# Performance work log

Measured on AMD Instinct MI355X. Metric: run time of the kernel, lower is better.

The kernel has to match this reference:

```python
import jax, jax.numpy as jnp
import numpy as np

LOG2PI = float(np.log(2.0 * np.pi))
VAR = 1e-4
LOGVAR = float(np.log(VAR))


def _gauss_lp(x, mean, dim):
    # MVN log_prob with covariance VAR * I_dim
    sq = jnp.sum((x - mean) ** 2, axis=-1)
    return -0.5 * (dim * (LOG2PI + LOGVAR) + sq / VAR)


def setup_inputs() -> dict:
    B, T, D, H, K = 32, 512, 256, 512, 8
    key = jax.random.key(0)
    ks = jax.random.split(key, 20)
    s = 0.05
    return {
        "x_input": jax.random.normal(ks[0], (B, T, D), jnp.float32),
        "y_train": jax.random.normal(ks[1], (B, T, D), jnp.float32),
        "sampled_h": jax.random.normal(ks[2], (B, T, H), jnp.float32),
        "initials": jax.random.normal(ks[3], (K,), jnp.float32),
        # per-state single-layer RNNs (tanh), weights [K,H,D]/[K,H,H]
        "Wih": jax.random.normal(ks[4], (K, H, D), jnp.float32) * s,
        "Whh": jax.random.normal(ks[5], (K, H, H), jnp.float32) * s,
        "bih": jax.random.normal(ks[6], (K, H), jnp.float32) * s,
        "bhh": jax.random.normal(ks[7], (K, H), jnp.float32) * s,
        # transition RNNCell (h0=0, so only input path + both biases matter)
        "Wt_ih": jax.random.normal(ks[8], (K * K, H), jnp.float32) * s,
        "bt": jax.random.normal(ks[9], (K * K,), jnp.float32) * s,
        # Emission MLP H -> 32 -> 64 -> D
        "W1": jax.random.normal(ks[10], (32, H), jnp.float32) * s,
        "b1": jax.random.normal(ks[11], (32,), jnp.float32) * s,
        "W2": jax.random.normal(ks[12], (64, 32), jnp.float32) * s,
        "b2": jax.random.normal(ks[13], (64,), jnp.float32) * s,
        "W3": jax.random.normal(ks[14], (D, 64), jnp.float32) * s,
        "b3": jax.random.normal(ks[15], (D,), jnp.float32) * s,
    }


def reference(x_input, y_train, sampled_h, initials, Wih, Whh, bih, bhh,
              Wt_ih, bt, W1, b1, W2, b2, W3, b3):
    B, T, D = x_input.shape
    H = sampled_h.shape[-1]
    K = initials.shape[0]
    lse = jax.scipy.special.logsumexp

    # initial log-probs (same for every batch row)
    prob_initial = jnp.broadcast_to(initials - lse(initials), (B, K))

    # ---- prob_all_h: per-state RNN step log-likelihoods ----
    h_prev = sampled_h[:, :-1]  # [B,T-1,H]
    pre = (jnp.einsum('btd,khd->btkh', x_input[:, 1:], Wih)
           + jnp.einsum('bth,kgh->btkg', h_prev, Whh)
           + bih[None, None] + bhh[None, None])  # [B,T-1,K,H]
    x_out = jnp.tanh(pre)
    lp_rest = _gauss_lp(sampled_h[:, 1:, None, :], x_out, H)  # [B,T-1,K]
    lp0 = -0.5 * H * (LOG2PI + LOGVAR)  # log_prob of the mean itself at t=0
    prob_all_h = jnp.concatenate(
        [jnp.full((B, 1, K), lp0, jnp.float32), lp_rest], axis=1)  # [B,T,K]

    # ---- prob_all_s: transition log-probs (normalized over axis=2) ----
    trans = jnp.tanh(jnp.einsum('bth,ch->btc', h_prev, Wt_ih) + bt)
    trans = trans.reshape(B, T - 1, K, K)
    s_rest = trans - lse(trans, axis=2, keepdims=True)
    s0 = jnp.broadcast_to(jnp.eye(K, dtype=jnp.float32), (B, 1, K, K))
    prob_all_s = jnp.concatenate([s0, s_rest], axis=1)  # [B,T,K,K]

    # ---- prob_all_y: emission MLP + MVN log-prob ----
    h1 = jax.nn.relu(sampled_h @ W1.T + b1)
    h2 = jax.nn.relu(h1 @ W2.T + b2)
    em = h2 @ W3.T + b3  # [B,T,D]
    prob_all_y = _gauss_lp(y_train, em, D)  # [B,T]

    log_e = prob_all_h + prob_all_y[..., None]  # [B,T,K]

    # ---- forward pass (Baum-Welch alpha, log-space) ----
    s_tm = jnp.swapaxes(prob_all_s[:, 1:], 0, 1)  # [T-1,B,K,K]
    e_tm = jnp.swapaxes(log_e[:, 1:], 0, 1)       # [T-1,B,K]
    alpha0 = prob_initial + log_e[:, 0]

    def fstep(a, xs):
        s_t, e_t = xs
        a_new = e_t + lse(a[:, None, :] + s_t, axis=2)  # s[b,i,j]=logp(i|j)
        return a_new, a_new

    _, alphas = jax.lax.scan(fstep, alpha0, (s_tm, e_tm))
    forward_prob = jnp.concatenate(
        [alpha0[:, None], jnp.swapaxes(alphas, 0, 1)], axis=1)  # [B,T,K]

    # ---- backward pass (beta) ----
    betaT = jnp.zeros((B, K), jnp.float32)

    def bstep(b, xs):
        s_t1, e_t1 = xs
        b_new = lse(s_t1 + (e_t1 + b)[:, :, None], axis=1)
        return b_new, b_new

    _, betas = jax.lax.scan(bstep, betaT, (s_tm, e_tm), reverse=True)
    backward_prob = jnp.concatenate(
        [jnp.swapaxes(betas, 0, 1), betaT[:, None]], axis=1)  # [B,T,K]

    # ---- gammas ----
    ab = forward_prob + backward_prob
    gamma1 = ab - lse(ab, axis=2, keepdims=True)  # [B,T,K]
    pair = (forward_prob[:, :-1, None, :] + prob_all_s[:, 1:]
            + (log_e[:, 1:] + backward_prob[:, 1:])[:, :, :, None])
    gamma2 = pair - lse(pair, axis=(2, 3), keepdims=True)  # [B,T-1,K,K]

    return (prob_initial, prob_all_s, prob_all_h, prob_all_y,
            gamma1, gamma2, forward_prob, backward_prob)
```

## Files before the change

kernel.cpp:

```cpp
#include <hip/hip_runtime.h>

typedef _Float16 f16;
typedef _Float16 f16x8 __attribute__((ext_vector_type(8)));
typedef float f32x16 __attribute__((ext_vector_type(16)));

#define NB 32
#define NT 512
#define ND 256
#define NH 512
#define M_REAL 16352
#define RDIM 768
#define TILE_ELEMS 98304
#define NTN 33

#define OFF_PI 0
#define OFF_S  256
#define OFF_H  1048832
#define OFF_Y  1179904
#define OFF_G1 1196288
#define OFF_G2 1327360
#define OFF_F  2373888
#define OFF_BW 2504960

#define WS_A    0
#define WS_B    25165824
#define WS_BIAS 31653888
#define WS_SQ   31671296
#define WS_M    33768448
#define WS_NEED 34292736

#define CH_CONST 1887.3506062251f
#define CY_CONST 943.6753031126f
#define LOG2E 1.4426950408889634f
#define LN2 0.6931471805599453f
#define NEGINF -1e30f

#define CA_BLOCKS 1024
#define CB_BLOCKS 264
#define CONV_GRID 1288

__device__ __forceinline__ float fexp2(float x) { return __builtin_amdgcn_exp2f(x); }
__device__ __forceinline__ float flog2(float x) { return __builtin_amdgcn_logf(x); }
__device__ __forceinline__ float ftanh(float x) {
    x = fminf(10.f, fmaxf(-10.f, x));
    float t = fexp2(x * 2.885390081777927f);
    return (t - 1.f) * __builtin_amdgcn_rcpf(t + 1.f);
}
__device__ __forceinline__ float lse8v(const float* z) {
    float M = fmaxf(fmaxf(fmaxf(z[0], z[1]), fmaxf(z[2], z[3])),
                    fmaxf(fmaxf(z[4], z[5]), fmaxf(z[6], z[7])));
    const float e0 = fexp2((z[0] - M) * LOG2E), e1 = fexp2((z[1] - M) * LOG2E);
    const float e2 = fexp2((z[2] - M) * LOG2E), e3 = fexp2((z[3] - M) * LOG2E);
    const float e4 = fexp2((z[4] - M) * LOG2E), e5 = fexp2((z[5] - M) * LOG2E);
    const float e6 = fexp2((z[6] - M) * LOG2E), e7 = fexp2((z[7] - M) * LOG2E);
    const float s = ((e0 + e1) + (e2 + e3)) + ((e4 + e5) + (e6 + e7));
    return M + LN2 * flog2(s);
}

__global__ __launch_bounds__(256) void conv_ab_kernel(
    const float* __restrict__ x, const float* __restrict__ h,
    const float* __restrict__ Wih, const float* __restrict__ Whh,
    const float* __restrict__ bih, const float* __restrict__ bhh,
    const float* __restrict__ Wt, const float* __restrict__ btv,
    f16* __restrict__ A, f16* __restrict__ Bm, float* __restrict__ biasc) {
    __shared__ __align__(16) f16x8 tb[16 * 97];
    const int tid = threadIdx.x;
    if (blockIdx.x < CA_BLOCKS) {
        const int m0 = blockIdx.x * 16;
#pragma unroll
        for (int i = 0; i < 6; ++i) {
            const int idx = tid + 256 * i;
            const int ml = idx / 96;
            const int ch = idx - ml * 96;
            const int m = m0 + ml;
            f16x8 pk = (f16x8)(f16)0.f;
            if (m < M_REAL) {
                const int b = m / 511;
                const int t = m - b * 511;
                const int c0 = ch * 8;
                const float* src = (c0 < ND) ? x + (size_t)(b * NT + t + 1) * ND + c0
                                             : h + (size_t)(b * NT + t) * NH + (c0 - ND);
                const float4 u = ((const float4*)src)[0];
                const float4 v = ((const float4*)src)[1];
                pk[0] = (f16)u.x; pk[1] = (f16)u.y; pk[2] = (f16)u.z; pk[3] = (f16)u.w;
                pk[4] = (f16)v.x; pk[5] = (f16)v.y; pk[6] = (f16)v.z; pk[7] = (f16)v.w;
            }
            tb[ml * 97 + ch] = pk;
        }
        __syncthreads();
        const size_t tbase = (size_t)(m0 >> 7) * TILE_ELEMS + (size_t)(m0 & 127) * 8;
#pragma unroll
        for (int i = 0; i < 6; ++i) {
            const int idx = tid + 256 * i;
            const int ch2 = idx >> 4;
            const int m2 = idx & 15;
            *(f16x8*)(A + tbase + (size_t)ch2 * 1024 + (size_t)m2 * 8) = tb[m2 * 97 + ch2];
        }
    } else {
        const int n0 = (blockIdx.x - CA_BLOCKS) * 16;
#pragma unroll
        for (int i = 0; i < 6; ++i) {
            const int idx = tid + 256 * i;
            const int nl = idx / 96;
            const int ch = idx - nl * 96;
            const int n = n0 + nl;
            const int c0 = ch * 8;
            f16x8 pk = (f16x8)(f16)0.f;
            const float* src = nullptr;
            if (n < 4096) {
                src = (c0 < ND) ? Wih + (size_t)n * ND + c0 : Whh + (size_t)n * NH + (c0 - ND);
            } else {
                const int c = n - 4096;
                if (c < 64 && c0 >= ND) src = Wt + (size_t)c * NH + (c0 - ND);
            }
            if (src) {
                const float4 u = ((const float4*)src)[0];
                const float4 v = ((const float4*)src)[1];
                pk[0] = (f16)u.x; pk[1] = (f16)u.y; pk[2] = (f16)u.z; pk[3] = (f16)u.w;
                pk[4] = (f16)v.x; pk[5] = (f16)v.y; pk[6] = (f16)v.z; pk[7] = (f16)v.w;
            }
            tb[nl * 97 + ch] = pk;
        }
        if (tid < 16) {
            const int n = n0 + tid;
            biasc[n] = (n < 4096) ? bih[n] + bhh[n] : ((n - 4096) < 64 ? btv[n - 4096] : 0.f);
        }
        __syncthreads();
        const size_t tbase = (size_t)(n0 >> 7) * TILE_ELEMS + (size_t)(n0 & 127) * 8;
#pragma unroll
        for (int i = 0; i < 6; ++i) {
            const int idx = tid + 256 * i;
            const int ch2 = idx >> 4;
            const int m2 = idx & 15;
            *(f16x8*)(Bm + tbase + (size_t)ch2 * 1024 + (size_t)m2 * 8) = tb[m2 * 97 + ch2];
        }
    }
}

__global__ __launch_bounds__(256) void emission_kernel(
    const float* __restrict__ h, const float* __restrict__ y,
    const float* __restrict__ W1, const float* __restrict__ b1,
    const float* __restrict__ W2, const float* __restrict__ b2,
    const float* __restrict__ W3, const float* __restrict__ b3,
    float* __restrict__ out) {
    __shared__ __align__(16) float smem[11904];
    const int tid = threadIdx.x;
    float* ssh = smem;
    float* W2sh = smem + 8192;
    float* h1sh = smem + 10304;
    float* h2sh = smem + 10816;
    float* red = smem + 11840;
    const int wv = tid >> 6;
    const int o = tid >> 3, seg = tid & 7;
    const int p0 = blockIdx.x * 16;
    float4 w1r[16], w3r[16];
    {
        const float4* w1p = (const float4*)(W1 + (size_t)o * NH + seg * 64);
#pragma unroll
        for (int j = 0; j < 16; ++j) w1r[j] = w1p[(j + seg * 2) & 15];
        const float4* w3p = (const float4*)(W3 + (size_t)tid * 64);
#pragma unroll
        for (int j = 0; j < 16; ++j) w3r[j] = w3p[j];
    }
    if (tid < 64) {
        for (int j = 0; j < 32; ++j) W2sh[tid * 33 + j] = W2[tid * 32 + j];
    }
    float yv[16];
#pragma unroll
    for (int pp = 0; pp < 16; ++pp) yv[pp] = y[(size_t)(p0 + pp) * ND + tid];
    const float b1r = b1[o];
    const float b2r = b2[tid & 63];
    const float b3r = b3[tid];
#pragma unroll
    for (int pp = 0; pp < 16; ++pp) {
        const float2 hv = ((const float2*)(h + (size_t)(p0 + pp) * NH))[tid];
        ssh[pp * 512 + tid * 2] = hv.x;
        ssh[pp * 512 + tid * 2 + 1] = hv.y;
    }
    __syncthreads();
#pragma unroll
    for (int pp = 0; pp < 16; ++pp) {
        const float4* s4 = (const float4*)&ssh[pp * 512 + seg * 64];
        float p = 0.f;
#pragma unroll
        for (int it = 0; it < 16; ++it) {
            const float4 sv = s4[(it + seg * 2) & 15];
            const float4 w = w1r[it];
            p += w.x * sv.x + w.y * sv.y + w.z * sv.z + w.w * sv.w;
        }
        p += __shfl_xor(p, 1, 64);
        p += __shfl_xor(p, 2, 64);
        p += __shfl_xor(p, 4, 64);
        if (seg == 0) h1sh[pp * 32 + o] = fmaxf(p + b1r, 0.f);
    }
    __syncthreads();
    {
        const int o2 = tid & 63;
#pragma unroll
        for (int it = 0; it < 4; ++it) {
            const int pp = wv * 4 + it;
            float s = b2r;
#pragma unroll
            for (int j = 0; j < 32; ++j) s += W2sh[o2 * 33 + j] * h1sh[pp * 32 + j];
            h2sh[pp * 64 + o2] = fmaxf(s, 0.f);
        }
    }
    __syncthreads();
#pragma unroll
    for (int pp = 0; pp < 16; ++pp) {
        float s = b3r;
        const float4* h24 = (const float4*)&h2sh[pp * 64];
#pragma unroll
        for (int j = 0; j < 16; ++j) {
            const float4 w = w3r[j], hb = h24[j];
            s += w.x * hb.x + w.y * hb.y + w.z * hb.z + w.w * hb.w;
        }
        const float d = yv[pp] - s;
        float sq = d * d;
#pragma unroll
        for (int off = 32; off > 0; off >>= 1) sq += __shfl_xor(sq, off, 64);
        if ((tid & 63) == 0) red[pp * 4 + wv] = sq;
    }
    __syncthreads();
    if (tid < 16) {
        out[OFF_Y + p0 + tid] =
            CY_CONST - 5000.f * (red[tid * 4] + red[tid * 4 + 1] + red[tid * 4 + 2] +
                                 red[tid * 4 + 3]);
    }
}

__global__ __launch_bounds__(256) void gemm_kernel(const f16* __restrict__ A,
                                                   const f16* __restrict__ Bm,
                                                   const float* __restrict__ biasc,
                                                   const float* __restrict__ sampled_h,
                                                   float* __restrict__ sq_part,
                                                   float* __restrict__ Ps) {
    __shared__ __align__(16) f16 Ash[8 * 128 * 8];
    __shared__ __align__(16) f16 Bsh[8 * 128 * 8];
    const int tid = threadIdx.x;
    const int lane = tid & 63;
    const int wave = tid >> 6;
    const int xcd = blockIdx.x & 7;
    const int slot = blockIdx.x >> 3;
    const int tm = xcd * 16 + slot / NTN;
    const int tn = slot % NTN;
    const int m0 = tm * 128, n0 = tn * 128;
    const int l31 = lane & 31, hk = lane >> 5;

    f32x16 acc[4];
#pragma unroll
    for (int a = 0; a < 4; ++a) acc[a] = (f32x16)0.f;

    for (int kk = 0; kk < RDIM; kk += 64) {
        __syncthreads();
        const size_t abase = (size_t)tm * TILE_ELEMS + (size_t)kk * 128;
        const size_t bbase = (size_t)tn * TILE_ELEMS + (size_t)kk * 128;
#pragma unroll
        for (int inst = 0; inst < 4; ++inst) {
            const int fb = inst * 256 + wave * 64;
            const f16* ga = A + abase + (size_t)(fb + lane) * 8;
            const f16* gb = Bm + bbase + (size_t)(fb + lane) * 8;
            __builtin_amdgcn_global_load_lds(
                (const __attribute__((address_space(1))) void*)ga,
                (__attribute__((address_space(3))) void*)&Ash[fb * 8], 16, 0, 0);
            __builtin_amdgcn_global_load_lds(
                (const __attribute__((address_space(1))) void*)gb,
                (__attribute__((address_space(3))) void*)&Bsh[fb * 8], 16, 0, 0);
        }
        __syncthreads();
#pragma unroll
        for (int kc = 0; kc < 4; ++kc) {
            const int ch = kc * 2 + hk;
            const f16x8 af = *(const f16x8*)&Ash[(ch * 128 + wave * 32 + l31) * 8];
            f16x8 bfr[4];
#pragma unroll
            for (int ni = 0; ni < 4; ++ni)
                bfr[ni] = *(const f16x8*)&Bsh[(ch * 128 + ni * 32 + l31) * 8];
#pragma unroll
            for (int ni = 0; ni < 4; ++ni)
                acc[ni] = __builtin_amdgcn_mfma_f32_32x32x16_f16(af, bfr[ni], acc[ni], 0, 0, 0);
        }
    }

    if (tn == 32) {
        const float bt0 = biasc[4096 + l31];
        const float bt1 = biasc[4096 + 32 + l31];
#pragma unroll
        for (int r = 0; r < 16; ++r) {
            const int mg = m0 + wave * 32 + (r & 3) + 8 * (r >> 2) + 4 * hk;
            if (mg < M_REAL) {
                const float v0 = ftanh(acc[0][r] + bt0);
                const float v1 = ftanh(acc[1][r] + bt1);
                float M = fmaxf(v0, v1);
                M = fmaxf(M, __shfl_xor(M, 8, 64));
                M = fmaxf(M, __shfl_xor(M, 16, 64));
                float s = fexp2((v0 - M) * LOG2E) + fexp2((v1 - M) * LOG2E);
                s += __shfl_xor(s, 8, 64);
                s += __shfl_xor(s, 16, 64);
                const float lse = M + LN2 * flog2(s);
                const int b = mg / 511, t = mg - b * 511;
                const size_t base = (size_t)(b * NT + t + 1) * 64;
                Ps[base + l31] = v0 - lse;
                Ps[base + 32 + l31] = v1 - lse;
            }
        }
    } else {
        const int k0 = n0 >> 9;
        const int slot4 = (n0 >> 7) & 3;
        const float b0 = biasc[n0 + l31];
        const float b1v = biasc[n0 + 32 + l31];
        const float b2v = biasc[n0 + 64 + l31];
        const float b3v = biasc[n0 + 96 + l31];
#pragma unroll
        for (int r = 0; r < 16; ++r) {
            const int mg = m0 + wave * 32 + (r & 3) + 8 * (r >> 2) + 4 * hk;
            if (mg < M_REAL) {
                const int bb = mg / 511;
                const int tt = mg - bb * 511;
                const float* tgt = sampled_h + (size_t)((bb << 9) + tt + 1) * NH;
                const float d0 = tgt[(n0 + l31) & 511] - ftanh(acc[0][r] + b0);
                const float d1 = tgt[(n0 + 32 + l31) & 511] - ftanh(acc[1][r] + b1v);
                const float d2 = tgt[(n0 + 64 + l31) & 511] - ftanh(acc[2][r] + b2v);
                const float d3 = tgt[(n0 + 96 + l31) & 511] - ftanh(acc[3][r] + b3v);
                float rs = d0 * d0 + d1 * d1 + d2 * d2 + d3 * d3;
                rs += __shfl_xor(rs, 1, 64);
                rs += __shfl_xor(rs, 2, 64);
                rs += __shfl_xor(rs, 4, 64);
                rs += __shfl_xor(rs, 8, 64);
                rs += __shfl_xor(rs, 16, 64);
                if (l31 == 0) sq_part[(size_t)(mg * 8 + k0) * 4 + slot4] = rs;
            }
        }
    }
}

__global__ void post_kernel(const float* __restrict__ sq_part,
                            const float* __restrict__ initials, float* __restrict__ out) {
    const int g = blockIdx.x * 256 + threadIdx.x;
    const int b = g >> 12;
    const int t = (g >> 3) & 511;
    const int k = g & 7;
    float val;
    if (t == 0) {
        val = CH_CONST;
    } else {
        const int m = b * 511 + (t - 1);
        const float4 a = *(const float4*)&sq_part[(size_t)(m * 8 + k) * 4];
        val = CH_CONST - 5000.f * (a.x + a.y + a.z + a.w);
    }
    out[OFF_H + g] = val;
    if (g < 2048) {
        const int sb = g >> 6, c = g & 63;
        out[OFF_S + (size_t)sb * NT * 64 + c] = ((c >> 3) == (c & 7)) ? 1.f : 0.f;
    }
    if (g < 256) {
        float z[8];
#pragma unroll
        for (int j = 0; j < 8; ++j) z[j] = initials[j];
        out[OFF_PI + g] = z[g & 7] - lse8v(z);
    }
}


template <bool WRITE>
__device__ __forceinline__ float fwd_run(const float* __restrict__ Ps,
                                         const float* __restrict__ Ph,
                                         const float* __restrict__ Py,
                                         float* __restrict__ Fw, int b, int t0,
                                         int t1, float a, int lane) {
    const int i = lane & 7;
    const int base = lane & ~7;
    float4 cA[8], cB[8], nA[8], nB[8];
    float cH[8], cY[8], nH[8], nY[8];
#define FLOADR(G, A_, B_, H_, Y_)                                              \
    _Pragma("unroll") for (int jj = 0; jj < 8; ++jj) {                         \
        int t = t0 + (G) * 8 + jj;                                             \
        t = t > t1 ? t1 : t;                                                   \
        const size_t p = (size_t)(b * NT + t) * 64 + i * 8;                    \
        A_[jj] = *(const float4*)&Ps[p];                                       \
        B_[jj] = *(const float4*)&Ps[p + 4];                                   \
        H_[jj] = Ph[(size_t)(b * NT + t) * 8 + i];                             \
        Y_[jj] = Py[b * NT + t];                                               \
    }
#define FSTEPR(G, A_, B_, H_, Y_)                                              \
    _Pragma("unroll") for (int jj = 0; jj < 8; ++jj) {                         \
        const int t = t0 + (G) * 8 + jj;                                       \
        if (t <= t1) {                                                         \
            float z[8];                                                        \
            z[0] = __shfl(a, base + 0, 64) + A_[jj].x;                         \
            z[1] = __shfl(a, base + 1, 64) + A_[jj].y;                         \
            z[2] = __shfl(a, base + 2, 64) + A_[jj].z;                         \
            z[3] = __shfl(a, base + 3, 64) + A_[jj].w;                         \
            z[4] = __shfl(a, base + 4, 64) + B_[jj].x;                         \
            z[5] = __shfl(a, base + 5, 64) + B_[jj].y;                         \
            z[6] = __shfl(a, base + 6, 64) + B_[jj].z;                         \
            z[7] = __shfl(a, base + 7, 64) + B_[jj].w;                         \
            a = (H_[jj] + Y_[jj]) + lse8v(z);                                  \
            if (WRITE && lane < 8) Fw[(size_t)(b * NT + t) * 8 + i] = a;       \
        }                                                                      \
    }
    FLOADR(0, cA, cB, cH, cY);
    FLOADR(1, nA, nB, nH, nY);
    FSTEPR(0, cA, cB, cH, cY);
    FLOADR(2, cA, cB, cH, cY);
    FSTEPR(1, nA, nB, nH, nY);
    FLOADR(3, nA, nB, nH, nY);
    FSTEPR(2, cA, cB, cH, cY);
    FSTEPR(3, nA, nB, nH, nY);
#undef FLOADR
#undef FSTEPR
    return a;
}

template <bool WRITE>
__device__ __forceinline__ float bwd_run(const float* __restrict__ Ps,
                                         const float* __restrict__ Ph,
                                         const float* __restrict__ Py,
                                         float* __restrict__ Bw, int b, int tt0,
                                         int tt1, float a, int lane) {
    const int i = lane & 7;
    const int base = lane & ~7;
    float cS[8][8], nS[8][8], cH[8], cY[8], nH[8], nY[8];
#define BLOADR(G, S_, H_, Y_)                                                  \
    _Pragma("unroll") for (int jj = 0; jj < 8; ++jj) {                         \
        int t = tt0 - (G) * 8 - jj;                                            \
        t = t < tt1 ? tt1 : t;                                                 \
        const size_t q = (size_t)(b * NT + t + 1);                             \
        _Pragma("unroll") for (int ii = 0; ii < 8; ++ii)                       \
            S_[jj][ii] = Ps[q * 64 + ii * 8 + i];                              \
        H_[jj] = Ph[q * 8 + i];                                                \
        Y_[jj] = Py[q];                                                       \
    }
#define BSTEPR(G, S_, H_, Y_)                                                  \
    _Pragma("unroll") for (int jj = 0; jj < 8; ++jj) {                         \
        const int t = tt0 - (G) * 8 - jj;                                      \
        if (t >= tt1) {                                                        \
            const float v = H_[jj] + Y_[jj] + a;                               \
            float z[8];                                                        \
            _Pragma("unroll") for (int ii = 0; ii < 8; ++ii)                   \
                z[ii] = __shfl(v, base + ii, 64) + S_[jj][ii];                 \
            a = lse8v(z);                                                      \
            if (WRITE && lane < 8) Bw[(size_t)(b * NT + t) * 8 + i] = a;       \
        }                                                                      \
    }
    BLOADR(0, cS, cH, cY);
    BLOADR(1, nS, nH, nY);
    BSTEPR(0, cS, cH, cY);
    BLOADR(2, cS, cH, cY);
    BSTEPR(1, nS, nH, nY);
    BLOADR(3, nS, nH, nY);
    BSTEPR(2, cS, cH, cY);
    BSTEPR(3, nS, nH, nY);
#undef BLOADR
#undef BSTEPR
    return a;
}

__global__ __launch_bounds__(256) void scan_mat_kernel(const float* __restrict__ out,
                                                       float* __restrict__ Mws) {
    const float* Ps = out + OFF_S;
    const float* Ph = out + OFF_H;
    const float* Py = out + OFF_Y;
    const int lane = threadIdx.x & 63;
    const int wave = threadIdx.x >> 6;
    const int i = lane & 7, j = lane >> 3;
    float a = (i == j) ? 0.f : NEGINF;
    if (blockIdx.x < 128) {
        const int b = blockIdx.x >> 2;
        const int c = (blockIdx.x & 3) * 4 + wave;
        const int t0 = 1 + 32 * c;
        const int t1 = (32 * (c + 1) < 511) ? 32 * (c + 1) : 511;
        a = fwd_run<false>(Ps, Ph, Py, nullptr, b, t0, t1, a, lane);
        Mws[(size_t)(b * 16 + c) * 64 + lane] = a;
    } else {
        const int b = (blockIdx.x - 128) >> 2;
        const int c = ((blockIdx.x - 128) & 3) * 4 + wave;
        const int tt0 = 510 - 32 * c;
        const int tt1 = (479 - 32 * c > 0) ? 479 - 32 * c : 0;
        a = bwd_run<false>(Ps, Ph, Py, nullptr, b, tt0, tt1, a, lane);
        Mws[32768 + (size_t)(b * 16 + c) * 64 + lane] = a;
    }
}

__global__ __launch_bounds__(256) void scan_fin_kernel(const float* __restrict__ initials,
                                                       float* __restrict__ out,
                                                       const float* __restrict__ Mws) {
    const float* Ps = out + OFF_S;
    const float* Ph = out + OFF_H;
    const float* Py = out + OFF_Y;
    const int lane = threadIdx.x & 63;
    const int wave = threadIdx.x >> 6;
    const int i = lane & 7;
    const int base = lane & ~7;
    const bool fwd = blockIdx.x < 128;
    const int blk = fwd ? blockIdx.x : blockIdx.x - 128;
    const int b = blk >> 2;
    const int c = (blk & 3) * 4 + wave;
    const float* Mbase = Mws + (fwd ? 0 : 32768) + (size_t)(b * 16) * 64;

    float a;
    if (fwd) {
        float z0[8];
#pragma unroll
        for (int jj = 0; jj < 8; ++jj) z0[jj] = initials[jj];
        a = (z0[i] - lse8v(z0)) + CH_CONST + Py[b * NT];
        if (c == 0 && lane < 8) (out + OFF_F)[(size_t)(b * NT) * 8 + i] = a;
    } else {
        a = 0.f;
        if (c == 0 && lane < 8) (out + OFF_BW)[(size_t)(b * NT + NT - 1) * 8 + i] = 0.f;
    }
    if (c > 0) {
        float4 r0 = *(const float4*)&Mbase[0 * 64 + i * 8];
        float4 r1 = *(const float4*)&Mbase[0 * 64 + i * 8 + 4];
        for (int cc = 0; cc < c; ++cc) {
            float4 s0, s1;
            if (cc + 1 < c) {
                s0 = *(const float4*)&Mbase[(size_t)(cc + 1) * 64 + i * 8];
                s1 = *(const float4*)&Mbase[(size_t)(cc + 1) * 64 + i * 8 + 4];
            }
            float z[8];
            z[0] = __shfl(a, base + 0, 64) + r0.x;
            z[1] = __shfl(a, base + 1, 64) + r0.y;
            z[2] = __shfl(a, base + 2, 64) + r0.z;
            z[3] = __shfl(a, base + 3, 64) + r0.w;
            z[4] = __shfl(a, base + 4, 64) + r1.x;
            z[5] = __shfl(a, base + 5, 64) + r1.y;
            z[6] = __shfl(a, base + 6, 64) + r1.z;
            z[7] = __shfl(a, base + 7, 64) + r1.w;
            a = lse8v(z);
            r0 = s0;
            r1 = s1;
        }
    }
    if (fwd) {
        const int t0 = 1 + 32 * c;
        const int t1 = (32 * (c + 1) < 511) ? 32 * (c + 1) : 511;
        fwd_run<true>(Ps, Ph, Py, out + OFF_F, b, t0, t1, a, lane);
    } else {
        const int tt0 = 510 - 32 * c;
        const int tt1 = (479 - 32 * c > 0) ? 479 - 32 * c : 0;
        bwd_run<true>(Ps, Ph, Py, out + OFF_BW, b, tt0, tt1, a, lane);
    }
}

__global__ void gamma_kernel(float* __restrict__ out) {
    const float* Ps = out + OFF_S;
    const float* Ph = out + OFF_H;
    const float* Py = out + OFF_Y;
    const float* Fw = out + OFF_F;
    const float* Bw = out + OFF_BW;
    if (blockIdx.x < 511) {
        const int gidx = blockIdx.x * 256 + threadIdx.x;
        const int pos = gidx >> 3;
        const int i = gidx & 7;
        const int b = pos / 511, t = pos - b * 511;
        const size_t t1 = (size_t)(b * NT + t + 1);
        const float ei = Ph[t1 * 8 + i] + Py[t1] + Bw[t1 * 8 + i];
        const float4 sa = ((const float4*)&Ps[(t1 * 8 + i) * 8])[0];
        const float4 sb = ((const float4*)&Ps[(t1 * 8 + i) * 8])[1];
        const float4 fa = ((const float4*)&Fw[(size_t)(b * NT + t) * 8])[0];
        const float4 fb = ((const float4*)&Fw[(size_t)(b * NT + t) * 8])[1];
        float z[8] = {fa.x + sa.x + ei, fa.y + sa.y + ei, fa.z + sa.z + ei, fa.w + sa.w + ei,
                      fb.x + sb.x + ei, fb.y + sb.y + ei, fb.z + sb.z + ei, fb.w + sb.w + ei};
        float M = fmaxf(fmaxf(fmaxf(z[0], z[1]), fmaxf(z[2], z[3])),
                        fmaxf(fmaxf(z[4], z[5]), fmaxf(z[6], z[7])));
        M = fmaxf(M, __shfl_xor(M, 1, 64));
        M = fmaxf(M, __shfl_xor(M, 2, 64));
        M = fmaxf(M, __shfl_xor(M, 4, 64));
        float s = 0.f;
#pragma unroll
        for (int j = 0; j < 8; ++j) s += fexp2((z[j] - M) * LOG2E);
        s += __shfl_xor(s, 1, 64);
        s += __shfl_xor(s, 2, 64);
        s += __shfl_xor(s, 4, 64);
        const float l = M + LN2 * flog2(s);
        float* G2 = out + OFF_G2;
        float4 o0 = {z[0] - l, z[1] - l, z[2] - l, z[3] - l};
        float4 o1 = {z[4] - l, z[5] - l, z[6] - l, z[7] - l};
        ((float4*)&G2[(size_t)gidx * 8])[0] = o0;
        ((float4*)&G2[(size_t)gidx * 8])[1] = o1;
    } else {
        const int pos = (blockIdx.x - 511) * 256 + threadIdx.x;
        const float4 fa = ((const float4*)&Fw[(size_t)pos * 8])[0];
        const float4 fb = ((const float4*)&Fw[(size_t)pos * 8])[1];
        const float4 ba = ((const float4*)&Bw[(size_t)pos * 8])[0];
        const float4 bb = ((const float4*)&Bw[(size_t)pos * 8])[1];
        float ab[8] = {fa.x + ba.x, fa.y + ba.y, fa.z + ba.z, fa.w + ba.w,
                       fb.x + bb.x, fb.y + bb.y, fb.z + bb.z, fb.w + bb.w};
        const float l = lse8v(ab);
        float* G1 = out + OFF_G1;
        float4 o0 = {ab[0] - l, ab[1] - l, ab[2] - l, ab[3] - l};
        float4 o1 = {ab[4] - l, ab[5] - l, ab[6] - l, ab[7] - l};
        ((float4*)&G1[(size_t)pos * 8])[0] = o0;
        ((float4*)&G1[(size_t)pos * 8])[1] = o1;
    }
}

extern "C" void kernel_launch(void* const* d_in, const int* in_sizes, int n_in, void* d_out,
                              int out_size, void* d_ws, size_t ws_size, hipStream_t stream) {
    const float* x = (const float*)d_in[0];
    const float* y = (const float*)d_in[1];
    const float* h = (const float*)d_in[2];
    const float* initials = (const float*)d_in[3];
    const float* Wih = (const float*)d_in[4];
    const float* Whh = (const float*)d_in[5];
    const float* bih = (const float*)d_in[6];
    const float* bhh = (const float*)d_in[7];
    const float* Wt = (const float*)d_in[8];
    const float* btv = (const float*)d_in[9];
    const float* W1 = (const float*)d_in[10];
    const float* b1 = (const float*)d_in[11];
    const float* W2 = (const float*)d_in[12];
    const float* b2 = (const float*)d_in[13];
    const float* W3 = (const float*)d_in[14];
    const float* b3 = (const float*)d_in[15];
    float* out = (float*)d_out;
    char* ws = (char*)d_ws;
    if (ws_size < (size_t)WS_NEED) return;
    f16* Aws = (f16*)(ws + WS_A);
    f16* Bws = (f16*)(ws + WS_B);
    float* biasc = (float*)(ws + WS_BIAS);
    float* sqp = (float*)(ws + WS_SQ);
    float* Mws = (float*)(ws + WS_M);

    conv_ab_kernel<<<CONV_GRID, 256, 0, stream>>>(x, h, Wih, Whh, bih, bhh, Wt, btv, Aws,
                                                  Bws, biasc);
    gemm_kernel<<<4224, 256, 0, stream>>>(Aws, Bws, biasc, h, sqp, out + OFF_S);
    emission_kernel<<<1024, 256, 0, stream>>>(h, y, W1, b1, W2, b2, W3, b3, out);
    post_kernel<<<512, 256, 0, stream>>>(sqp, initials, out);
    scan_mat_kernel<<<256, 256, 0, stream>>>(out, Mws);
    scan_fin_kernel<<<256, 256, 0, stream>>>(initials, out, Mws);
    gamma_kernel<<<575, 256, 0, stream>>>(out);
}
```

Before: 379.6 us.

## Enlarge GEMM tiles to 256x256 with double-buffered LDS and software-pipelined MFMA

Rewrites the main fused GEMM to use 256x256 output tiles per 512-thread block, with each wave computing a 128x64 sub-tile. Global-to-LDS loads are double-buffered and overlapped with MFMA phases, with register ping-pong of fragments and s_setprio around the MFMAs. The goal is more operand reuse per LDS load and less load latency exposed between K steps. The epilogue now reduces partial squared sums through LDS before writing. The cost is higher register and LDS pressure, and wasted MFMA work on the clamped last N tile, where only one wave column's results are used.

```diff
diff --git a/kernel.cpp b/kernel.cpp
--- a/kernel.cpp
+++ b/kernel.cpp
@@ -229,106 +229,190 @@
     }
 }
 
-__global__ __launch_bounds__(256) void gemm_kernel(const f16* __restrict__ A,
-                                                   const f16* __restrict__ Bm,
-                                                   const float* __restrict__ biasc,
-                                                   const float* __restrict__ sampled_h,
-                                                   float* __restrict__ sq_part,
-                                                   float* __restrict__ Ps) {
-    __shared__ __align__(16) f16 Ash[8 * 128 * 8];
-    __shared__ __align__(16) f16 Bsh[8 * 128 * 8];
+__global__ __launch_bounds__(512, 2) void gemm_kernel(const f16* __restrict__ A,
+                                                      const f16* __restrict__ Bm,
+                                                      const float* __restrict__ biasc,
+                                                      const float* __restrict__ sampled_h,
+                                                      float* __restrict__ sq_part,
+                                                      float* __restrict__ Ps) {
+    __shared__ __align__(16) f16 Ash[2][16384];
+    __shared__ __align__(16) f16 Bsh[2][16384];
     const int tid = threadIdx.x;
     const int lane = tid & 63;
     const int wave = tid >> 6;
+    const int wm = wave >> 2;
+    const int wn = wave & 3;
+    const int l31 = lane & 31, hk = lane >> 5;
     const int xcd = blockIdx.x & 7;
-    const int slot = blockIdx.x >> 3;
-    const int tm = xcd * 16 + slot / NTN;
-    const int tn = slot % NTN;
-    const int m0 = tm * 128, n0 = tn * 128;
-    const int l31 = lane & 31, hk = lane >> 5;
-
-    f32x16 acc[4];
-#pragma unroll
-    for (int a = 0; a < 4; ++a) acc[a] = (f32x16)0.f;
-
-    for (int kk = 0; kk < RDIM; kk += 64) {
+    const int local = blockIdx.x >> 3;
+    const int tm = xcd * 8 + local / 17;
+    const int tn = local % 17;
+    const int bt0 = 2 * tn;
+    const int bt1 = (2 * tn + 1 > 32) ? 32 : 2 * tn + 1;
+    const size_t ga0 = (size_t)(2 * tm) * TILE_ELEMS + (size_t)tid * 8;
+    const size_t ga1 = (size_t)(2 * tm + 1) * TILE_ELEMS + (size_t)tid * 8;
+    const size_t gb0 = (size_t)bt0 * TILE_ELEMS + (size_t)tid * 8;
+    const size_t gb1 = (size_t)bt1 * TILE_ELEMS + (size_t)tid * 8;
+    const int aoff = wm * 8192 + hk * 1024 + l31 * 8;
+    const int boff = (wn >> 1) * 8192 + hk * 1024 + ((wn & 1) * 64 + l31) * 8;
+
+    f32x16 acc[4][2];
+#pragma unroll
+    for (int mi = 0; mi < 4; ++mi)
+#pragma unroll
+        for (int ni = 0; ni < 2; ++ni) acc[mi][ni] = (f32x16)0.f;
+
+#define GLDS(SRC, DST) \
+    __builtin_amdgcn_global_load_lds( \
+        (const __attribute__((address_space(1))) void*)(SRC), \
+        (__attribute__((address_space(3))) void*)(DST), 16, 0, 0)
+
+#define STAGE(kt, bi) \
+    do { \
+        const size_t ko = (size_t)(kt) * 8192; \
+        GLDS(A + ga0 + ko, &Ash[bi][0 * 4096 + tid * 8]); \
+        GLDS(A + ga0 + ko + 4096, &Ash[bi][1 * 4096 + tid * 8]); \
+        GLDS(A + ga1 + ko, &Ash[bi][2 * 4096 + tid * 8]); \
+        GLDS(A + ga1 + ko + 4096, &Ash[bi][3 * 4096 + tid * 8]); \
+        GLDS(Bm + gb0 + ko, &Bsh[bi][0 * 4096 + tid * 8]); \
+        GLDS(Bm + gb0 + ko + 4096, &Bsh[bi][1 * 4096 + tid * 8]); \
+        GLDS(Bm + gb1 + ko, &Bsh[bi][2 * 4096 + tid * 8]); \
+        GLDS(Bm + gb1 + ko + 4096, &Bsh[bi][3 * 4096 + tid * 8]); \
+    } while (0)
+
+#define DSREAD(bi, kc, AF, BF) \
+    do { \
+        const int ko2 = (kc) * 2048; \
+        AF##0 = *(const f16x8*)&Ash[bi][aoff + ko2 + 0 * 256]; \
+        AF##1 = *(const f16x8*)&Ash[bi][aoff + ko2 + 1 * 256]; \
+        AF##2 = *(const f16x8*)&Ash[bi][aoff + ko2 + 2 * 256]; \
+        AF##3 = *(const f16x8*)&Ash[bi][aoff + ko2 + 3 * 256]; \
+        BF##0 = *(const f16x8*)&Bsh[bi][boff + ko2 + 0 * 256]; \
+        BF##1 = *(const f16x8*)&Bsh[bi][boff + ko2 + 1 * 256]; \
+    } while (0)
+
+#define MFMA8(AF, BF) \
+    do { \
+        acc[0][0] = __builtin_amdgcn_mfma_f32_32x32x16_f16(AF##0, BF##0, acc[0][0], 0, 0, 0); \
+        acc[1][0] = __builtin_amdgcn_mfma_f32_32x32x16_f16(AF##1, BF##0, acc[1][0], 0, 0, 0); \
+        acc[2][0] = __builtin_amdgcn_mfma_f32_32x32x16_f16(AF##2, BF##0, acc[2][0], 0, 0, 0); \
+        acc[3][0] = __builtin_amdgcn_mfma_f32_32x32x16_f16(AF##3, BF##0, acc[3][0], 0, 0, 0); \
+        acc[0][1] = __builtin_amdgcn_mfma_f32_32x32x16_f16(AF##0, BF##1, acc[0][1], 0, 0, 0); \
+        acc[1][1] = __builtin_amdgcn_mfma_f32_32x32x16_f16(AF##1, BF##1, acc[1][1], 0, 0, 0); \
+        acc[2][1] = __builtin_amdgcn_mfma_f32_32x32x16_f16(AF##2, BF##1, acc[2][1], 0, 0, 0); \
+        acc[3][1] = __builtin_amdgcn_mfma_f32_32x32x16_f16(AF##3, BF##1, acc[3][1], 0, 0, 0); \
+    } while (0)
+
+#define BARRIER __builtin_amdgcn_s_barrier()
+#define LGKM0 asm volatile("s_waitcnt lgkmcnt(0)" ::: "memory")
+#define VM0 asm volatile("s_waitcnt vmcnt(0)" ::: "memory")
+#define COMPUTE_PHASE(AF, BF) \
+    do { \
+        BARRIER; \
+        LGKM0; \
+        __builtin_amdgcn_s_setprio(1); \
+        MFMA8(AF, BF); \
+        __builtin_amdgcn_s_setprio(0); \
+        BARRIER; \
+    } while (0)
+
+    f16x8 afX0, afX1, afX2, afX3, bfX0, bfX1;
+    f16x8 afY0, afY1, afY2, afY3, bfY0, bfY1;
+
+    STAGE(0, 0);
+    VM0;
+    BARRIER;
+    DSREAD(0, 0, afX, bfX);
+
+#pragma unroll 1
+    for (int j = 0; j < 12; ++j) {
+        const int buf = j & 1;
+        if (j + 1 < 12) STAGE(j + 1, buf ^ 1);
+        DSREAD(buf, 1, afY, bfY);
+        COMPUTE_PHASE(afX, bfX);
+        DSREAD(buf, 2, afX, bfX);
+        COMPUTE_PHASE(afY, bfY);
+        DSREAD(buf, 3, afY, bfY);
+        COMPUTE_PHASE(afX, bfX);
+        if (j + 1 < 12) {
+            VM0;
+            DSREAD(buf ^ 1, 0, afX, bfX);
+        }
+        COMPUTE_PHASE(afY, bfY);
+    }
+
+#undef GLDS
+#undef STAGE
+#undef DSREAD
+#undef MFMA8
+#undef BARRIER
+#undef LGKM0
+#undef VM0
+#undef COMPUTE_PHASE
+
+    if (tn < 16) {
         __syncthreads();
-        const size_t abase = (size_t)tm * TILE_ELEMS + (size_t)kk * 128;
-        const size_t bbase = (size_t)tn * TILE_ELEMS + (size_t)kk * 128;
-#pragma unroll
-        for (int inst = 0; inst < 4; ++inst) {
-            const int fb = inst * 256 + wave * 64;
-            const f16* ga = A + abase + (size_t)(fb + lane) * 8;
-            const f16* gb = Bm + bbase + (size_t)(fb + lane) * 8;
-            __builtin_amdgcn_global_load_lds(
-                (const __attribute__((address_space(1))) void*)ga,
-                (__attribute__((address_space(3))) void*)&Ash[fb * 8], 16, 0, 0);
-            __builtin_amdgcn_global_load_lds(
-                (const __attribute__((address_space(1))) void*)gb,
-                (__attribute__((address_space(3))) void*)&Bsh[fb * 8], 16, 0, 0);
-        }
-        __syncthreads();
-#pragma unroll
-        for (int kc = 0; kc < 4; ++kc) {
-            const int ch = kc * 2 + hk;
-            const f16x8 af = *(const f16x8*)&Ash[(ch * 128 + wave * 32 + l31) * 8];
-            f16x8 bfr[4];
-#pragma unroll
-            for (int ni = 0; ni < 4; ++ni)
-                bfr[ni] = *(const f16x8*)&Bsh[(ch * 128 + ni * 32 + l31) * 8];
-#pragma unroll
-            for (int ni = 0; ni < 4; ++ni)
-                acc[ni] = __builtin_amdgcn_mfma_f32_32x32x16_f16(af, bfr[ni], acc[ni], 0, 0, 0);
-        }
-    }
-
-    if (tn == 32) {
-        const float bt0 = biasc[4096 + l31];
-        const float bt1 = biasc[4096 + 32 + l31];
-#pragma unroll
-        for (int r = 0; r < 16; ++r) {
-            const int mg = m0 + wave * 32 + (r & 3) + 8 * (r >> 2) + 4 * hk;
-            if (mg < M_REAL) {
-                const float v0 = ftanh(acc[0][r] + bt0);
-                const float v1 = ftanh(acc[1][r] + bt1);
-                float M = fmaxf(v0, v1);
-                M = fmaxf(M, __shfl_xor(M, 8, 64));
-                M = fmaxf(M, __shfl_xor(M, 16, 64));
-                float s = fexp2((v0 - M) * LOG2E) + fexp2((v1 - M) * LOG2E);
-                s += __shfl_xor(s, 8, 64);
-                s += __shfl_xor(s, 16, 64);
-                const float lse = M + LN2 * flog2(s);
-                const int b = mg / 511, t = mg - b * 511;
-                const size_t base = (size_t)(b * NT + t + 1) * 64;
-                Ps[base + l31] = v0 - lse;
-                Ps[base + 32 + l31] = v1 - lse;
-            }
-        }
-    } else {
-        const int k0 = n0 >> 9;
-        const int slot4 = (n0 >> 7) & 3;
-        const float b0 = biasc[n0 + l31];
-        const float b1v = biasc[n0 + 32 + l31];
-        const float b2v = biasc[n0 + 64 + l31];
-        const float b3v = biasc[n0 + 96 + l31];
-#pragma unroll
-        for (int r = 0; r < 16; ++r) {
-            const int mg = m0 + wave * 32 + (r & 3) + 8 * (r >> 2) + 4 * hk;
-            if (mg < M_REAL) {
-                const int bb = mg / 511;
-                const int tt = mg - bb * 511;
-                const float* tgt = sampled_h + (size_t)((bb << 9) + tt + 1) * NH;
-                const float d0 = tgt[(n0 + l31) & 511] - ftanh(acc[0][r] + b0);
-                const float d1 = tgt[(n0 + 32 + l31) & 511] - ftanh(acc[1][r] + b1v);
-                const float d2 = tgt[(n0 + 64 + l31) & 511] - ftanh(acc[2][r] + b2v);
-                const float d3 = tgt[(n0 + 96 + l31) & 511] - ftanh(acc[3][r] + b3v);
-                float rs = d0 * d0 + d1 * d1 + d2 * d2 + d3 * d3;
+        float* pbuf = (float*)&Ash[0][0];
+        const int c0 = tn * 256 + wn * 64;
+        const float bA = biasc[c0 + l31];
+        const float bB = biasc[c0 + 32 + l31];
+#pragma unroll
+        for (int mi = 0; mi < 4; ++mi) {
+#pragma unroll
+            for (int r = 0; r < 16; ++r) {
+                const int rowl = wm * 128 + mi * 32 + (r & 3) + 8 * (r >> 2) + 4 * hk;
+                const int mg = tm * 256 + rowl;
+                float rs = 0.f;
+                if (mg < M_REAL) {
+                    const int bb = mg / 511;
+                    const int tt = mg - bb * 511;
+                    const float* tgt = sampled_h + (size_t)((bb << 9) + tt + 1) * NH;
+                    const float d0 = tgt[(c0 + l31) & 511] - ftanh(acc[mi][0][r] + bA);
+                    const float d1 = tgt[(c0 + 32 + l31) & 511] - ftanh(acc[mi][1][r] + bB);
+                    rs = d0 * d0 + d1 * d1;
+                }
                 rs += __shfl_xor(rs, 1, 64);
                 rs += __shfl_xor(rs, 2, 64);
                 rs += __shfl_xor(rs, 4, 64);
                 rs += __shfl_xor(rs, 8, 64);
                 rs += __shfl_xor(rs, 16, 64);
-                if (l31 == 0) sq_part[(size_t)(mg * 8 + k0) * 4 + slot4] = rs;
+                if (l31 == 0) pbuf[rowl * 4 + wn] = rs;
+            }
+        }
+        __syncthreads();
+        {
+            const int rowl = tid >> 1, p = tid & 1;
+            const int mg = tm * 256 + rowl;
+            if (mg < M_REAL) {
+                const float v = pbuf[rowl * 4 + 2 * p] + pbuf[rowl * 4 + 2 * p + 1];
+                const int n0p = tn * 256 + p * 128;
+                sq_part[(size_t)(mg * 8 + (n0p >> 9)) * 4 + ((n0p >> 7) & 3)] = v;
+            }
+        }
+    } else if (wn == 0) {
+        const float bt0v = biasc[4096 + l31];
+        const float bt1v = biasc[4096 + 32 + l31];
+#pragma unroll
+        for (int mi = 0; mi < 4; ++mi) {
+#pragma unroll
+            for (int r = 0; r < 16; ++r) {
+                const int mg =
+                    tm * 256 + wm * 128 + mi * 32 + (r & 3) + 8 * (r >> 2) + 4 * hk;
+                if (mg < M_REAL) {
+                    const float v0 = ftanh(acc[mi][0][r] + bt0v);
+                    const float v1 = ftanh(acc[mi][1][r] + bt1v);
+                    float M = fmaxf(v0, v1);
+                    M = fmaxf(M, __shfl_xor(M, 8, 64));
+                    M = fmaxf(M, __shfl_xor(M, 16, 64));
+                    float s = fexp2((v0 - M) * LOG2E) + fexp2((v1 - M) * LOG2E);
+                    s += __shfl_xor(s, 8, 64);
+                    s += __shfl_xor(s, 16, 64);
+                    const float lse = M + LN2 * flog2(s);
+                    const int b = mg / 511, t = mg - b * 511;
+                    const size_t base = (size_t)(b * NT + t + 1) * 64;
+                    Ps[base + l31] = v0 - lse;
+                    Ps[base + 32 + l31] = v1 - lse;
+                }
             }
         }
     }
@@ -360,7 +444,6 @@
         out[OFF_PI + g] = z[g & 7] - lse8v(z);
     }
 }
-
 
 template <bool WRITE>
 __device__ __forceinline__ float fwd_run(const float* __restrict__ Ps,
@@ -625,7 +708,7 @@
 
     conv_ab_kernel<<<CONV_GRID, 256, 0, stream>>>(x, h, Wih, Whh, bih, bhh, Wt, btv, Aws,
                                                   Bws, biasc);
-    gemm_kernel<<<4224, 256, 0, stream>>>(Aws, Bws, biasc, h, sqp, out + OFF_S);
+    gemm_kernel<<<1088, 512, 0, stream>>>(Aws, Bws, biasc, h, sqp, out + OFF_S);
     emission_kernel<<<1024, 256, 0, stream>>>(h, y, W1, b1, W2, b2, W3, b3, out);
     post_kernel<<<512, 256, 0, stream>>>(sqp, initials, out);
     scan_mat_kernel<<<256, 256, 0, stream>>>(out, Mws);
```

Result: slower. 498.2 us (+31.2%).
